# Kernel tuning notes

Measured on AMD Instinct MI355X. Metric: run time of the kernel, lower is better.

## Reference

```python
import jax, jax.numpy as jnp
from jax import lax
import numpy as np

B, C, H, W = 32, 128, 32, 32
ZDIM = 256
KH = KW = 3
NB_UNITS = C * C * KH * KW  # 147456
BN_EPS = 1e-6


def setup_inputs() -> dict:
    key = jax.random.key(0)
    ks = jax.random.split(key, 5)
    x = jax.random.normal(ks[0], (B, C, H, W), dtype=jnp.float32)
    z = jax.random.normal(ks[1], (B, ZDIM), dtype=jnp.float32)
    # glorot-uniform Dense kernel
    limit = np.sqrt(6.0 / (ZDIM + NB_UNITS)).astype(np.float32)
    dense_w = jax.random.uniform(ks[2], (ZDIM, NB_UNITS), dtype=jnp.float32,
                                 minval=-limit, maxval=limit)
    dense_b = jnp.zeros((NB_UNITS,), dtype=jnp.float32)
    # gamma initialized to +/- 0.02 (scale_for_weights)
    sign = jnp.where(jax.random.bernoulli(ks[3], 0.5, (NB_UNITS,)), 1.0, -1.0)
    gamma = (0.02 * sign).astype(jnp.float32)
    beta = jnp.zeros((NB_UNITS,), dtype=jnp.float32)
    b = jnp.zeros((C,), dtype=jnp.float32)  # deconv bias (zeros in original)
    return {"x": x, "z": z, "dense_w": dense_w, "dense_b": dense_b,
            "gamma": gamma, "beta": beta, "b": b}


def _per_sample_deconv(xi, wi):
    # xi: (C,H,W); wi: (C_in=stack, C_out=filter, KH, KW)
    # out[f,p,q] = sum_{s,u,v} xi[s, p+u-1, q+v-1] * wi[s,f,u,v]
    k = jnp.transpose(wi, (1, 0, 2, 3))  # OIHW: (f, s, u, v)
    y = lax.conv_general_dilated(xi[None], k, window_strides=(1, 1),
                                 padding=[(1, 1), (1, 1)],
                                 dimension_numbers=("NCHW", "OIHW", "NCHW"))
    return y[0]


def reference(x, z, dense_w, dense_b, gamma, beta, b):
    # hypernetwork: Dense(relu) -> BatchNorm(axis=1, batch stats) -> Reshape
    h = jax.nn.relu(z @ dense_w + dense_b)            # (B, NB_UNITS)
    mean = jnp.mean(h, axis=0)
    std = jnp.sqrt(jnp.var(h, axis=0))
    h = (h - mean) / (std + BN_EPS)
    h = gamma * h + beta
    Wk = h.reshape(B, C, C, KH, KW)                   # per-sample kernels (s,f,u,v)
    out = jax.vmap(_per_sample_deconv)(x, Wk)         # (B, C, H, W)
    out = out + b[None, :, None, None]
    return out + x                                    # residual add
```

## Files before the change

### kernel.cpp

```cpp
#include <hip/hip_runtime.h>

#define NB 147456
#define NB2 73728
#define ZD 256
#define BSZ 32
#define CCH 128

typedef __attribute__((ext_vector_type(8))) short short8;
typedef __attribute__((ext_vector_type(16))) float floatx16;

__device__ __forceinline__ unsigned short f2bf(float f) {
    unsigned int u = __float_as_uint(f);
    return (unsigned short)((u + 0x7fffu + ((u >> 16) & 1u)) >> 16);
}

__global__ __launch_bounds__(128) void hyper_gemm_bn(
    const float* __restrict__ z, const float* __restrict__ dw,
    const float* __restrict__ db, const float* __restrict__ gamma,
    const float* __restrict__ beta, unsigned short* __restrict__ wkn)
{
    __shared__ float zs[ZD * BSZ];
    int t = threadIdx.x;
    {
        const float4* z4 = (const float4*)z;
        float4* zw = (float4*)zs;
#pragma unroll
        for (int i = 0; i < 16; i++) zw[t + i * 128] = z4[t + i * 128];
    }
    __syncthreads();

    int n0 = (blockIdx.x * 128 + t) * 2;
    size_t nc = (size_t)(n0 >> 1);
    const float2* dw2 = (const float2*)dw;

    float acc0[32], acc1[32];
#pragma unroll
    for (int b = 0; b < 32; b++) { acc0[b] = 0.f; acc1[b] = 0.f; }

    const float4* zs4 = (const float4*)zs;
    float2 wc[16], wn[16];
#pragma unroll
    for (int j = 0; j < 16; j++) wc[j] = dw2[(size_t)j * NB2 + nc];

    for (int c = 0; c < 16; c++) {
        if (c < 15) {
#pragma unroll
            for (int j = 0; j < 16; j++)
                wn[j] = dw2[(size_t)(c * 16 + 16 + j) * NB2 + nc];
        }
#pragma unroll
        for (int b = 0; b < 32; b++) {
            float4 z0 = zs4[b * 64 + c * 4 + 0];
            float4 z1 = zs4[b * 64 + c * 4 + 1];
            float4 z2 = zs4[b * 64 + c * 4 + 2];
            float4 z3 = zs4[b * 64 + c * 4 + 3];
            float zv[16] = { z0.x, z0.y, z0.z, z0.w, z1.x, z1.y, z1.z, z1.w,
                             z2.x, z2.y, z2.z, z2.w, z3.x, z3.y, z3.z, z3.w };
#pragma unroll
            for (int j = 0; j < 16; j++) {
                acc0[b] += zv[j] * wc[j].x;
                acc1[b] += zv[j] * wc[j].y;
            }
        }
#pragma unroll
        for (int j = 0; j < 16; j++) wc[j] = wn[j];
    }

    float bias0 = db[n0], bias1 = db[n0 + 1];
    float s0 = 0.f, q0 = 0.f, s1 = 0.f, q1 = 0.f;
#pragma unroll
    for (int b = 0; b < 32; b++) {
        float h0 = fmaxf(acc0[b] + bias0, 0.f); acc0[b] = h0; s0 += h0; q0 += h0 * h0;
        float h1 = fmaxf(acc1[b] + bias1, 0.f); acc1[b] = h1; s1 += h1; q1 += h1 * h1;
    }
    float m0 = s0 * (1.f/32.f), m1 = s1 * (1.f/32.f);
    float v0 = fmaxf(q0 * (1.f/32.f) - m0 * m0, 0.f);
    float v1 = fmaxf(q1 * (1.f/32.f) - m1 * m1, 0.f);
    float sc0 = gamma[n0]     / (sqrtf(v0) + 1e-6f), bt0 = beta[n0];
    float sc1 = gamma[n0 + 1] / (sqrtf(v1) + 1e-6f), bt1 = beta[n0 + 1];

    unsigned int* wout = (unsigned int*)wkn;
#pragma unroll
    for (int b = 0; b < 32; b++) {
        float w0 = sc0 * (acc0[b] - m0) + bt0;
        float w1 = sc1 * (acc1[b] - m1) + bt1;
        wout[((size_t)b * NB + n0) >> 1] = (unsigned int)f2bf(w0) | ((unsigned int)f2bf(w1) << 16);
    }
}

__global__ __launch_bounds__(256) void repack(
    const unsigned short* __restrict__ wkn, unsigned short* __restrict__ wkt)
{
    __shared__ unsigned int lt[16 * 580];
    int t = threadIdx.x;
    int b = blockIdx.x;
    int s0 = blockIdx.y * 16;
    const unsigned int* src = (const unsigned int*)wkn + ((size_t)b * NB >> 1) + (size_t)s0 * 576;
#pragma unroll
    for (int i = 0; i < 36; i++) {
        int idx = t + i * 256;
        int si = idx / 576;
        int j2 = idx - si * 576;
        lt[si * 580 + j2] = src[(size_t)si * 576 + j2];
    }
    __syncthreads();
    const unsigned short* ls = (const unsigned short*)lt;
#pragma unroll
    for (int i = 0; i < 9; i++) {
        int tau = t + i * 256;
        int half = tau & 1;
        int unit = tau >> 1;
        int uv = unit >> 7;
        int f = unit & 127;
        int col = f * 9 + uv;
        unsigned short v[8];
#pragma unroll
        for (int ss = 0; ss < 8; ss++)
            v[ss] = ls[(half * 8 + ss) * 1160 + col];
        uint4 o;
        o.x = v[0] | ((unsigned)v[1] << 16);
        o.y = v[2] | ((unsigned)v[3] << 16);
        o.z = v[4] | ((unsigned)v[5] << 16);
        o.w = v[6] | ((unsigned)v[7] << 16);
        ((uint4*)wkt)[((((size_t)b * 9 + uv) * 128 + f) * 16) + (s0 >> 3) + half] = o;
    }
}

__global__ __launch_bounds__(256) void x_transpose(
    const float* __restrict__ x, unsigned short* __restrict__ xb16)
{
    __shared__ unsigned short lx[32 * 130];
    int t = threadIdx.x;
    int p = blockIdx.x;
    int b = blockIdx.y;
    const float* xp = x + (size_t)b * CCH * 1024 + p * 32;
#pragma unroll
    for (int i = 0; i < 16; i++) {
        int idx = t + i * 256;
        int s = idx >> 5;
        int q = idx & 31;
        lx[q * 130 + s] = f2bf(xp[(size_t)s * 1024 + q]);
    }
    __syncthreads();
#pragma unroll
    for (int i = 0; i < 2; i++) {
        int tau = t + i * 256;
        int q = tau >> 4;
        int ch = tau & 15;
        const unsigned short* r = &lx[q * 130 + ch * 8];
        uint4 o;
        o.x = r[0] | ((unsigned)r[1] << 16);
        o.y = r[2] | ((unsigned)r[3] << 16);
        o.z = r[4] | ((unsigned)r[5] << 16);
        o.w = r[6] | ((unsigned)r[7] << 16);
        ((uint4*)xb16)[((((size_t)b * 32 + p) * 32) + q) * 16 + ch] = o;
    }
}

__global__ __launch_bounds__(128) void conv_mfma(
    const float* __restrict__ x, const unsigned short* __restrict__ xb16,
    const unsigned short* __restrict__ wkt, const float* __restrict__ cb,
    float* __restrict__ out)
{
    __shared__ short8 lds8[4 * 34 * 17];
    int t = threadIdx.x;
    int p0 = blockIdx.x * 2;
    int b = blockIdx.y;
    int lane = t & 63;
    int fbase = (t >> 6) * 64;
    int qcol = lane & 31;
    int klane = lane >> 5;

    {
        int r = t >> 5;
        int col = ((t >> 4) & 1) ? 33 : 0;
        int ch = t & 15;
        short8 zz = { 0, 0, 0, 0, 0, 0, 0, 0 };
        lds8[(r * 34 + col) * 17 + ch] = zz;
    }
    const uint4* xsrc = (const uint4*)xb16;
#pragma unroll
    for (int i = 0; i < 16; i++) {
        int tau = t + i * 128;
        int ch = tau & 15;
        int q = (tau >> 4) & 31;
        int r = tau >> 9;
        int prow = p0 - 1 + r;
        uint4 v = make_uint4(0, 0, 0, 0);
        if (prow >= 0 && prow < 32)
            v = xsrc[((((size_t)b * 32 + prow) * 32) + q) * 16 + ch];
        *(uint4*)&lds8[(r * 34 + q + 1) * 17 + ch] = v;
    }
    __syncthreads();

    floatx16 acc[2][2];
#pragma unroll
    for (int mi = 0; mi < 2; mi++)
#pragma unroll
        for (int ni = 0; ni < 2; ni++)
#pragma unroll
            for (int r = 0; r < 16; r++) acc[mi][ni][r] = 0.f;

    const short8* A8 = (const short8*)wkt;
#pragma unroll
    for (int u = 0; u < 3; u++)
#pragma unroll
    for (int v = 0; v < 3; v++) {
        int uvi = u * 3 + v;
        const short8* Au = A8 + ((size_t)(b * 9 + uvi) << 11);
#pragma unroll
        for (int ks = 0; ks < 8; ks++) {
            int koff = ks * 2 + klane;
            short8 a0 = Au[(fbase + qcol) * 16 + koff];
            short8 a1 = Au[(fbase + 32 + qcol) * 16 + koff];
            short8 b0 = lds8[(u * 34 + qcol + v) * 17 + koff];
            short8 b1 = lds8[((u + 1) * 34 + qcol + v) * 17 + koff];
            acc[0][0] = __builtin_amdgcn_mfma_f32_32x32x16_bf16(a0, b0, acc[0][0], 0, 0, 0);
            acc[0][1] = __builtin_amdgcn_mfma_f32_32x32x16_bf16(a0, b1, acc[0][1], 0, 0, 0);
            acc[1][0] = __builtin_amdgcn_mfma_f32_32x32x16_bf16(a1, b0, acc[1][0], 0, 0, 0);
            acc[1][1] = __builtin_amdgcn_mfma_f32_32x32x16_bf16(a1, b1, acc[1][1], 0, 0, 0);
        }
    }

    const size_t xb = (size_t)b * CCH * 1024;
#pragma unroll
    for (int mi = 0; mi < 2; mi++)
#pragma unroll
    for (int ni = 0; ni < 2; ni++) {
        int p = p0 + ni;
#pragma unroll
        for (int r = 0; r < 16; r++) {
            int fl = (r & 3) + 8 * (r >> 2) + 4 * klane;
            int f = fbase + mi * 32 + fl;
            size_t idx = xb + (size_t)f * 1024 + p * 32 + qcol;
            out[idx] = acc[mi][ni][r] + x[idx] + cb[f];
        }
    }
}

extern "C" void kernel_launch(void* const* d_in, const int* in_sizes, int n_in,
                              void* d_out, int out_size, void* d_ws, size_t ws_size,
                              hipStream_t stream) {
    const float* x     = (const float*)d_in[0];
    const float* z     = (const float*)d_in[1];
    const float* dw    = (const float*)d_in[2];
    const float* db    = (const float*)d_in[3];
    const float* gamma = (const float*)d_in[4];
    const float* beta  = (const float*)d_in[5];
    const float* cb    = (const float*)d_in[6];
    float* out = (float*)d_out;

    unsigned short* wkn = (unsigned short*)d_ws;
    unsigned short* wkt = (unsigned short*)((char*)d_ws + (size_t)BSZ * NB * 2);
    unsigned short* xb16 = wkn;

    hyper_gemm_bn<<<NB / 256, 128, 0, stream>>>(z, dw, db, gamma, beta, wkn);
    repack<<<dim3(BSZ, 8), 256, 0, stream>>>(wkn, wkt);
    x_transpose<<<dim3(32, BSZ), 256, 0, stream>>>(x, xb16);
    conv_mfma<<<dim3(16, BSZ), 128, 0, stream>>>(x, xb16, wkt, cb, out);
}
```

Baseline: 307.4 us.

## Fuse repack and x transpose, remap conv blocks to XCDs, reuse LDS rows

The dense GEMM loop now double-buffers weight loads explicitly with two register banks instead of copying next-to-current each chunk. The weight repack and x transpose kernels merge into one launch, and xb16 gets its own workspace region so the two can run together. The conv grid is flattened and remapped so each XCD handles a contiguous set of batches for L2 locality. The conv loop is reordered so the four LDS input rows are loaded once per (v,ks) and reused across u, cutting LDS reads. The cost is higher register pressure in the GEMM and a larger workspace.

```diff
diff --git a/kernel.cpp b/kernel.cpp
--- a/kernel.cpp
+++ b/kernel.cpp
@@ -38,33 +38,42 @@
     for (int b = 0; b < 32; b++) { acc0[b] = 0.f; acc1[b] = 0.f; }
 
     const float4* zs4 = (const float4*)zs;
-    float2 wc[16], wn[16];
-#pragma unroll
-    for (int j = 0; j < 16; j++) wc[j] = dw2[(size_t)j * NB2 + nc];
-
-    for (int c = 0; c < 16; c++) {
-        if (c < 15) {
+    float2 wa[16], wb[16];
+#pragma unroll
+    for (int j = 0; j < 16; j++) wa[j] = dw2[(size_t)j * NB2 + nc];
+
+#define FMA_CHUNK(CC, WBUF)                                              \
+    {                                                                    \
+        _Pragma("unroll")                                                \
+        for (int b = 0; b < 32; b++) {                                   \
+            float4 z0 = zs4[b * 64 + (CC) * 4 + 0];                      \
+            float4 z1 = zs4[b * 64 + (CC) * 4 + 1];                      \
+            float4 z2 = zs4[b * 64 + (CC) * 4 + 2];                      \
+            float4 z3 = zs4[b * 64 + (CC) * 4 + 3];                      \
+            float zv[16] = { z0.x, z0.y, z0.z, z0.w, z1.x, z1.y, z1.z,   \
+                             z1.w, z2.x, z2.y, z2.z, z2.w, z3.x, z3.y,   \
+                             z3.z, z3.w };                               \
+            _Pragma("unroll")                                            \
+            for (int j = 0; j < 16; j++) {                               \
+                acc0[b] += zv[j] * WBUF[j].x;                            \
+                acc1[b] += zv[j] * WBUF[j].y;                            \
+            }                                                            \
+        }                                                                \
+    }
+
+    for (int c = 0; c < 16; c += 2) {
+#pragma unroll
+        for (int j = 0; j < 16; j++)
+            wb[j] = dw2[(size_t)((c + 1) * 16 + j) * NB2 + nc];
+        FMA_CHUNK(c, wa)
+        if (c + 2 < 16) {
 #pragma unroll
             for (int j = 0; j < 16; j++)
-                wn[j] = dw2[(size_t)(c * 16 + 16 + j) * NB2 + nc];
-        }
-#pragma unroll
-        for (int b = 0; b < 32; b++) {
-            float4 z0 = zs4[b * 64 + c * 4 + 0];
-            float4 z1 = zs4[b * 64 + c * 4 + 1];
-            float4 z2 = zs4[b * 64 + c * 4 + 2];
-            float4 z3 = zs4[b * 64 + c * 4 + 3];
-            float zv[16] = { z0.x, z0.y, z0.z, z0.w, z1.x, z1.y, z1.z, z1.w,
-                             z2.x, z2.y, z2.z, z2.w, z3.x, z3.y, z3.z, z3.w };
-#pragma unroll
-            for (int j = 0; j < 16; j++) {
-                acc0[b] += zv[j] * wc[j].x;
-                acc1[b] += zv[j] * wc[j].y;
-            }
-        }
-#pragma unroll
-        for (int j = 0; j < 16; j++) wc[j] = wn[j];
-    }
+                wa[j] = dw2[(size_t)((c + 2) * 16 + j) * NB2 + nc];
+        }
+        FMA_CHUNK(c + 1, wb)
+    }
+#undef FMA_CHUNK
 
     float bias0 = db[n0], bias1 = db[n0 + 1];
     float s0 = 0.f, q0 = 0.f, s1 = 0.f, q1 = 0.f;
@@ -88,72 +97,72 @@
     }
 }
 
-__global__ __launch_bounds__(256) void repack(
-    const unsigned short* __restrict__ wkn, unsigned short* __restrict__ wkt)
-{
-    __shared__ unsigned int lt[16 * 580];
-    int t = threadIdx.x;
-    int b = blockIdx.x;
-    int s0 = blockIdx.y * 16;
-    const unsigned int* src = (const unsigned int*)wkn + ((size_t)b * NB >> 1) + (size_t)s0 * 576;
-#pragma unroll
-    for (int i = 0; i < 36; i++) {
-        int idx = t + i * 256;
-        int si = idx / 576;
-        int j2 = idx - si * 576;
-        lt[si * 580 + j2] = src[(size_t)si * 576 + j2];
-    }
-    __syncthreads();
-    const unsigned short* ls = (const unsigned short*)lt;
-#pragma unroll
-    for (int i = 0; i < 9; i++) {
-        int tau = t + i * 256;
-        int half = tau & 1;
-        int unit = tau >> 1;
-        int uv = unit >> 7;
-        int f = unit & 127;
-        int col = f * 9 + uv;
-        unsigned short v[8];
-#pragma unroll
-        for (int ss = 0; ss < 8; ss++)
-            v[ss] = ls[(half * 8 + ss) * 1160 + col];
-        uint4 o;
-        o.x = v[0] | ((unsigned)v[1] << 16);
-        o.y = v[2] | ((unsigned)v[3] << 16);
-        o.z = v[4] | ((unsigned)v[5] << 16);
-        o.w = v[6] | ((unsigned)v[7] << 16);
-        ((uint4*)wkt)[((((size_t)b * 9 + uv) * 128 + f) * 16) + (s0 >> 3) + half] = o;
-    }
-}
-
-__global__ __launch_bounds__(256) void x_transpose(
+__global__ __launch_bounds__(256) void repack_xt(
+    const unsigned short* __restrict__ wkn, unsigned short* __restrict__ wkt,
     const float* __restrict__ x, unsigned short* __restrict__ xb16)
 {
-    __shared__ unsigned short lx[32 * 130];
+    __shared__ char lmem[16 * 580 * 4];
     int t = threadIdx.x;
-    int p = blockIdx.x;
-    int b = blockIdx.y;
-    const float* xp = x + (size_t)b * CCH * 1024 + p * 32;
-#pragma unroll
-    for (int i = 0; i < 16; i++) {
-        int idx = t + i * 256;
-        int s = idx >> 5;
-        int q = idx & 31;
-        lx[q * 130 + s] = f2bf(xp[(size_t)s * 1024 + q]);
-    }
-    __syncthreads();
-#pragma unroll
-    for (int i = 0; i < 2; i++) {
-        int tau = t + i * 256;
-        int q = tau >> 4;
-        int ch = tau & 15;
-        const unsigned short* r = &lx[q * 130 + ch * 8];
-        uint4 o;
-        o.x = r[0] | ((unsigned)r[1] << 16);
-        o.y = r[2] | ((unsigned)r[3] << 16);
-        o.z = r[4] | ((unsigned)r[5] << 16);
-        o.w = r[6] | ((unsigned)r[7] << 16);
-        ((uint4*)xb16)[((((size_t)b * 32 + p) * 32) + q) * 16 + ch] = o;
+    if (blockIdx.x < 256) {
+        unsigned int* lt = (unsigned int*)lmem;
+        int b = blockIdx.x >> 3;
+        int s0 = (blockIdx.x & 7) * 16;
+        const unsigned int* src = (const unsigned int*)wkn + ((size_t)b * NB >> 1) + (size_t)s0 * 576;
+#pragma unroll
+        for (int i = 0; i < 36; i++) {
+            int idx = t + i * 256;
+            int si = idx / 576;
+            int j2 = idx - si * 576;
+            lt[si * 580 + j2] = src[(size_t)si * 576 + j2];
+        }
+        __syncthreads();
+        const unsigned short* ls = (const unsigned short*)lt;
+#pragma unroll
+        for (int i = 0; i < 9; i++) {
+            int tau = t + i * 256;
+            int half = tau & 1;
+            int unit = tau >> 1;
+            int uv = unit >> 7;
+            int f = unit & 127;
+            int col = f * 9 + uv;
+            unsigned short v[8];
+#pragma unroll
+            for (int ss = 0; ss < 8; ss++)
+                v[ss] = ls[(half * 8 + ss) * 1160 + col];
+            uint4 o;
+            o.x = v[0] | ((unsigned)v[1] << 16);
+            o.y = v[2] | ((unsigned)v[3] << 16);
+            o.z = v[4] | ((unsigned)v[5] << 16);
+            o.w = v[6] | ((unsigned)v[7] << 16);
+            ((uint4*)wkt)[((((size_t)b * 9 + uv) * 128 + f) * 16) + (s0 >> 3) + half] = o;
+        }
+    } else {
+        unsigned short* lx = (unsigned short*)lmem;
+        int idx = blockIdx.x - 256;
+        int p = idx & 31;
+        int b = idx >> 5;
+        const float* xp = x + (size_t)b * CCH * 1024 + p * 32;
+#pragma unroll
+        for (int i = 0; i < 16; i++) {
+            int ii = t + i * 256;
+            int s = ii >> 5;
+            int q = ii & 31;
+            lx[q * 130 + s] = f2bf(xp[(size_t)s * 1024 + q]);
+        }
+        __syncthreads();
+#pragma unroll
+        for (int i = 0; i < 2; i++) {
+            int tau = t + i * 256;
+            int q = tau >> 4;
+            int ch = tau & 15;
+            const unsigned short* r = &lx[q * 130 + ch * 8];
+            uint4 o;
+            o.x = r[0] | ((unsigned)r[1] << 16);
+            o.y = r[2] | ((unsigned)r[3] << 16);
+            o.z = r[4] | ((unsigned)r[5] << 16);
+            o.w = r[6] | ((unsigned)r[7] << 16);
+            ((uint4*)xb16)[((((size_t)b * 32 + p) * 32) + q) * 16 + ch] = o;
+        }
     }
 }
 
@@ -164,8 +173,11 @@
 {
     __shared__ short8 lds8[4 * 34 * 17];
     int t = threadIdx.x;
-    int p0 = blockIdx.x * 2;
-    int b = blockIdx.y;
+    int w = blockIdx.x;
+    int xcd = w & 7;
+    int slot = w >> 3;
+    int b = (xcd << 2) | (slot >> 4);
+    int p0 = (slot & 15) * 2;
     int lane = t & 63;
     int fbase = (t >> 6) * 64;
     int qcol = lane & 31;
@@ -201,24 +213,25 @@
 #pragma unroll
             for (int r = 0; r < 16; r++) acc[mi][ni][r] = 0.f;
 
-    const short8* A8 = (const short8*)wkt;
-#pragma unroll
-    for (int u = 0; u < 3; u++)
-#pragma unroll
-    for (int v = 0; v < 3; v++) {
-        int uvi = u * 3 + v;
-        const short8* Au = A8 + ((size_t)(b * 9 + uvi) << 11);
-#pragma unroll
-        for (int ks = 0; ks < 8; ks++) {
-            int koff = ks * 2 + klane;
+    const short8* A8 = (const short8*)wkt + ((size_t)b * 9 << 11);
+#pragma unroll
+    for (int v = 0; v < 3; v++)
+#pragma unroll
+    for (int ks = 0; ks < 8; ks++) {
+        int koff = ks * 2 + klane;
+        short8 br[4];
+#pragma unroll
+        for (int r = 0; r < 4; r++)
+            br[r] = lds8[(r * 34 + qcol + v) * 17 + koff];
+#pragma unroll
+        for (int u = 0; u < 3; u++) {
+            const short8* Au = A8 + ((size_t)(u * 3 + v) << 11);
             short8 a0 = Au[(fbase + qcol) * 16 + koff];
             short8 a1 = Au[(fbase + 32 + qcol) * 16 + koff];
-            short8 b0 = lds8[(u * 34 + qcol + v) * 17 + koff];
-            short8 b1 = lds8[((u + 1) * 34 + qcol + v) * 17 + koff];
-            acc[0][0] = __builtin_amdgcn_mfma_f32_32x32x16_bf16(a0, b0, acc[0][0], 0, 0, 0);
-            acc[0][1] = __builtin_amdgcn_mfma_f32_32x32x16_bf16(a0, b1, acc[0][1], 0, 0, 0);
-            acc[1][0] = __builtin_amdgcn_mfma_f32_32x32x16_bf16(a1, b0, acc[1][0], 0, 0, 0);
-            acc[1][1] = __builtin_amdgcn_mfma_f32_32x32x16_bf16(a1, b1, acc[1][1], 0, 0, 0);
+            acc[0][0] = __builtin_amdgcn_mfma_f32_32x32x16_bf16(a0, br[u],     acc[0][0], 0, 0, 0);
+            acc[0][1] = __builtin_amdgcn_mfma_f32_32x32x16_bf16(a0, br[u + 1], acc[0][1], 0, 0, 0);
+            acc[1][0] = __builtin_amdgcn_mfma_f32_32x32x16_bf16(a1, br[u],     acc[1][0], 0, 0, 0);
+            acc[1][1] = __builtin_amdgcn_mfma_f32_32x32x16_bf16(a1, br[u + 1], acc[1][1], 0, 0, 0);
         }
     }
 
@@ -250,12 +263,11 @@
     const float* cb    = (const float*)d_in[6];
     float* out = (float*)d_out;
 
-    unsigned short* wkn = (unsigned short*)d_ws;
-    unsigned short* wkt = (unsigned short*)((char*)d_ws + (size_t)BSZ * NB * 2);
-    unsigned short* xb16 = wkn;
+    unsigned short* wkn  = (unsigned short*)d_ws;
+    unsigned short* wkt  = (unsigned short*)((char*)d_ws + (size_t)BSZ * NB * 2);
+    unsigned short* xb16 = (unsigned short*)((char*)d_ws + (size_t)BSZ * NB * 4);
 
     hyper_gemm_bn<<<NB / 256, 128, 0, stream>>>(z, dw, db, gamma, beta, wkn);
-    repack<<<dim3(BSZ, 8), 256, 0, stream>>>(wkn, wkt);
-    x_transpose<<<dim3(32, BSZ), 256, 0, stream>>>(x, xb16);
-    conv_mfma<<<dim3(16, BSZ), 128, 0, stream>>>(x, xb16, wkt, cb, out);
-}
+    repack_xt<<<256 + 1024, 256, 0, stream>>>(wkn, wkt, x, xb16);
+    conv_mfma<<<512, 128, 0, stream>>>(x, xb16, wkt, cb, out);
+}
```

Measured after the change: 334.1 us. 1.09x slower.
